# Performance work log

Hardware: AMD Instinct MI355X
Metric: run time of the kernel (lower is better)

The kernel has to match this reference:

```python
import jax, jax.numpy as jnp
import numpy as np

N = 1_000_000   # total points
C = 20          # semantic classes
B = 4           # scenes in batch
L = 200         # instance label vocabulary
INST = 64       # number of proposals/instances
M = 300_000     # masked points (len(object_idxs))
T = 320_000     # total proposal rows
IGNORE = -100
PREPARE_EPOCHS = 128


def setup_inputs() -> dict:
    key = jax.random.key(0)
    ks = jax.random.split(key, 12)
    semantic_scores = jax.random.normal(ks[0], (N, C), jnp.float32)
    semantic_labels = jax.random.randint(ks[1], (N,), 0, C)
    lab = jax.random.randint(ks[2], (N,), 0, L)
    ign = jax.random.uniform(ks[3], (N,)) < 0.05
    instance_labels = jnp.where(ign, IGNORE, lab)
    pt_offsets = jax.random.normal(ks[4], (N, 3), jnp.float32)
    instance_info = jax.random.normal(ks[5], (N, 9), jnp.float32)
    coords = jax.random.normal(ks[6], (N, 3), jnp.float32)
    mask_logits = jax.random.normal(ks[7], (INST, M), jnp.float32)
    object_idxs = jax.random.randint(ks[8], (M,), 0, N)
    col1 = jax.random.randint(ks[9], (T,), 0, N)
    proposals_idx_shift = jnp.stack([jnp.zeros_like(col1), col1], axis=1)
    mids = jnp.sort(jax.random.randint(ks[10], (INST - 1,), 0, T))
    proposals_offset_shift = jnp.concatenate(
        [jnp.zeros((1,), jnp.int32), mids.astype(jnp.int32), jnp.full((1,), T, jnp.int32)])
    inst_batch_ids = jax.random.randint(ks[11], (INST,), 0, B)
    batch_offsets = jnp.array([0, N // 4, N // 2, 3 * N // 4, N], dtype=jnp.int32)
    batch_ids = jnp.clip(jnp.searchsorted(batch_offsets, object_idxs, side='right') - 1, 0, B - 1)
    inst_pred_seg_label = jax.random.randint(jax.random.fold_in(key, 99), (INST,), 0, C)
    return dict(semantic_scores=semantic_scores, pt_offsets=pt_offsets,
                instance_info=instance_info, coords=coords, mask_logits=mask_logits,
                semantic_labels=semantic_labels, instance_labels=instance_labels,
                object_idxs=object_idxs, proposals_idx_shift=proposals_idx_shift,
                proposals_offset_shift=proposals_offset_shift, inst_batch_ids=inst_batch_ids,
                batch_ids=batch_ids, batch_offsets=batch_offsets,
                inst_pred_seg_label=inst_pred_seg_label, epoch=200)


def reference(semantic_scores, pt_offsets, instance_info, coords, mask_logits,
              semantic_labels, instance_labels, object_idxs, proposals_idx_shift,
              proposals_offset_shift, inst_batch_ids, batch_ids, batch_offsets,
              inst_pred_seg_label, epoch):
    f32 = jnp.float32
    n_pts = semantic_scores.shape[0]
    n_inst, m_pts = mask_logits.shape
    n_batch = batch_offsets.shape[0] - 1
    LW = L + 1  # label buckets, bucket 0 == ignore(-100)

    # --- semantic cross entropy (ignore_index) ---
    logp = jax.nn.log_softmax(semantic_scores, axis=-1)
    sem_valid = semantic_labels != IGNORE
    safe_lab = jnp.where(sem_valid, semantic_labels, 0)
    nll = -jnp.take_along_axis(logp, safe_lab[:, None], axis=1)[:, 0]
    semantic_loss = jnp.sum(nll * sem_valid) / jnp.maximum(jnp.sum(sem_valid), 1)

    # --- offset losses ---
    gt_offsets = instance_info[:, 0:3] - coords
    pt_dist = jnp.sum(jnp.abs(pt_offsets - gt_offsets), axis=-1)
    valid = (instance_labels != IGNORE).astype(f32)
    vsum = jnp.sum(valid) + 1e-6
    offset_norm_loss = jnp.sum(pt_dist * valid) / vsum
    gt_u = gt_offsets / (jnp.linalg.norm(gt_offsets, axis=1, keepdims=True) + 1e-8)
    pt_u = pt_offsets / (jnp.linalg.norm(pt_offsets, axis=1, keepdims=True) + 1e-8)
    offset_dir_loss = jnp.sum(-jnp.sum(gt_u * pt_u, axis=-1) * valid) / vsum

    loss = semantic_loss + offset_norm_loss + offset_dir_loss

    if epoch > PREPARE_EPOCHS:
        # map instance labels to ids: ignore -> 0, label l -> l+1 (order-preserving, so
        # argmax-first tie-break == torch.mode smallest-value tie-break)
        labels_id = jnp.where(instance_labels == IGNORE, 0, instance_labels + 1)
        # segment id per proposal row from CSR offsets
        seg = jnp.clip(jnp.searchsorted(proposals_offset_shift, jnp.arange(T), side='right') - 1,
                       0, n_inst - 1)
        prop_lab = labels_id[proposals_idx_shift[:, 1]]
        hist = jax.ops.segment_sum(jnp.ones((T,), f32), seg * LW + prop_lab,
                                   num_segments=n_inst * LW).reshape(n_inst, LW)
        mode_id = jnp.argmax(hist, axis=1)                       # [INST] per-instance mode vote

        masked_lab = labels_id[object_idxs]                      # [M]
        sem_masked = semantic_labels[object_idxs]                # [M]
        skip = (mode_id == 0) | (inst_pred_seg_label <= 3)       # [INST]

        batch_match = inst_batch_ids[:, None] == batch_ids[None, :]           # [INST,M]
        sem_match = inst_pred_seg_label[:, None] == sem_masked[None, :]       # [INST,M]
        weights = batch_match.astype(f32) * jnp.where(skip[:, None], 1.0,
                                                      sem_match.astype(f32))  # [INST,M]

        # per-batch label histograms (full points and masked points)
        point_batch = jnp.clip(jnp.searchsorted(batch_offsets, jnp.arange(n_pts),
                                                side='right') - 1, 0, n_batch - 1)
        hist_full = jax.ops.segment_sum(jnp.ones((n_pts,), f32), point_batch * LW + labels_id,
                                        num_segments=n_batch * LW).reshape(n_batch, LW)
        hist_mask = jax.ops.segment_sum(jnp.ones((m_pts,), f32), batch_ids * LW + masked_lab,
                                        num_segments=n_batch * LW).reshape(n_batch, LW)
        num = hist_mask[inst_batch_ids, mode_id]
        den = hist_full[inst_batch_ids, mode_id]
        cover = jnp.where(den > 0, num / den, 0.0)
        pos = (~skip) & (cover > 0.3)
        inst_gt_mask = (pos[:, None] & (masked_lab[None, :] == mode_id[:, None])).astype(f32)

        pred = jax.nn.sigmoid(mask_logits)
        wb = (weights > 0).astype(f32)
        inter = jnp.sum(wb * pred * inst_gt_mask, axis=1)
        union = jnp.sum(wb * pred * pred, axis=1) + jnp.sum(wb * inst_gt_mask * inst_gt_mask, axis=1) + 1e-5
        dice_n = 1.0 - 2.0 * inter / union
        dice_valid = (~skip) & (jnp.sum(wb, axis=1) > 0)
        dice_loss = jnp.sum(jnp.where(dice_valid, dice_n, 0.0)) / (jnp.sum(dice_valid.astype(f32)) + 1e-6)

        # BCE(sigmoid(x), t) in stable form: softplus(x) - t*x
        bce = jax.nn.softplus(mask_logits) - inst_gt_mask * mask_logits
        score_loss = jnp.sum(bce * weights) / (jnp.sum(weights) + 1e-6)

        loss = loss + score_loss + dice_loss
    return loss
```

## Files before the change

kernel.cpp:

```cpp
#include <hip/hip_runtime.h>
#include <math.h>

namespace {

constexpr int N_PTS  = 1000000;
constexpr int C_CLS  = 20;
constexpr int N_B    = 4;
constexpr int L_LAB  = 200;
constexpr int LW     = L_LAB + 1;
constexpr int N_INST = 64;
constexpr int M_PTS  = 300000;
constexpr int T_PROP = 320000;
constexpr int IGN    = -100;
constexpr int PREP   = 128;

constexpr size_t OFF_G      = 0;
constexpr size_t OFF_INTER  = 64;
constexpr size_t OFF_UP     = 576;
constexpr size_t OFF_UG     = 1088;
constexpr size_t OFF_WBS    = 1600;
constexpr size_t OFF_SN     = 2112;
constexpr size_t OFF_HFULL  = 2624;
constexpr size_t OFF_HMASK  = 5840;
constexpr size_t OFF_IHIST  = 9056;
constexpr size_t OFF_FLAGS  = 60512;
constexpr size_t ZERO_BYTES = 60768;
constexpr size_t OFF_META   = 60800;
constexpr size_t WS_REQUIRED = OFF_META + (size_t)M_PTS * 2;

__device__ __forceinline__ float waveSumF(float v) {
  #pragma unroll
  for (int off = 32; off > 0; off >>= 1) v += __shfl_down(v, off, 64);
  return v;
}
__device__ __forceinline__ int waveMaxI(int v) {
  #pragma unroll
  for (int off = 32; off > 0; off >>= 1) v = max(v, __shfl_down(v, off, 64));
  return v;
}

constexpr int PB_PT   = 1024;
constexpr int PB_HF   = 256;
constexpr int PB_PROP = 256;
constexpr int PB_HM   = 256;
constexpr int A_BLOCKS = PB_PT + PB_HF + PB_PROP + PB_HM;

__global__ __launch_bounds__(256) void k_A(const float* __restrict__ scores,
                                           const float* __restrict__ pt_off,
                                           const float* __restrict__ info,
                                           const float* __restrict__ coords,
                                           const int* __restrict__ sem_lab,
                                           const int* __restrict__ inst_lab,
                                           const int* __restrict__ obj_idx,
                                           const int* __restrict__ batch_ids,
                                           const int* __restrict__ prop_idx,
                                           const int* __restrict__ prop_off,
                                           const int* __restrict__ batch_off,
                                           double* __restrict__ g,
                                           int* __restrict__ hist_full,
                                           int* __restrict__ hist_mask,
                                           int* __restrict__ inst_hist,
                                           unsigned short* __restrict__ meta,
                                           int write_meta) {
  __shared__ int sh[N_B * LW];
  const int bx = blockIdx.x;

  if (bx < PB_PT) {
    float s_nll = 0.f, s_cnt = 0.f, s_dist = 0.f, s_dir = 0.f, s_val = 0.f;
    const int gid = bx * blockDim.x + threadIdx.x;
    const int p0  = gid * 4;
    if (p0 < N_PTS) {
      const int4 sl4 = *reinterpret_cast<const int4*>(sem_lab + p0);
      const int4 il4 = *reinterpret_cast<const int4*>(inst_lab + p0);
      const float4* c4 = reinterpret_cast<const float4*>(coords + (size_t)p0 * 3);
      const float4 ca = c4[0], cb = c4[1], cc = c4[2];
      const float4* o4 = reinterpret_cast<const float4*>(pt_off + (size_t)p0 * 3);
      const float4 oa = o4[0], ob = o4[1], oc = o4[2];
      const float4* i4 = reinterpret_cast<const float4*>(info + (size_t)p0 * 9);
      const float4 f0 = i4[0], f2 = i4[2], f4 = i4[4], f5 = i4[5], f6 = i4[6], f7 = i4[7];
      const float cx[4] = { ca.x, ca.w, cb.z, cc.y };
      const float cy[4] = { ca.y, cb.x, cb.w, cc.z };
      const float cz[4] = { ca.z, cb.y, cc.x, cc.w };
      const float ox[4] = { oa.x, oa.w, ob.z, oc.y };
      const float oy[4] = { oa.y, ob.x, ob.w, oc.z };
      const float oz[4] = { oa.z, ob.y, oc.x, oc.w };
      const float ix[4] = { f0.x, f2.y, f4.z, f6.w };
      const float iy[4] = { f0.y, f2.z, f4.w, f7.x };
      const float iz[4] = { f0.z, f2.w, f5.x, f7.y };
      const int sl[4] = { sl4.x, sl4.y, sl4.z, sl4.w };
      const int il[4] = { il4.x, il4.y, il4.z, il4.w };
      #pragma unroll
      for (int k = 0; k < 4; ++k) {
        const int p = p0 + k;
        const float4* r4 = reinterpret_cast<const float4*>(scores + (size_t)p * C_CLS);
        float x[C_CLS];
        #pragma unroll
        for (int q = 0; q < C_CLS / 4; ++q) {
          const float4 v = r4[q];
          x[4 * q + 0] = v.x; x[4 * q + 1] = v.y; x[4 * q + 2] = v.z; x[4 * q + 3] = v.w;
        }
        float mx = x[0];
        #pragma unroll
        for (int c = 1; c < C_CLS; ++c) mx = fmaxf(mx, x[c]);
        float se = 0.f;
        #pragma unroll
        for (int c = 0; c < C_CLS; ++c) se += __expf(x[c] - mx);
        const float lse = mx + __logf(se);
        if (sl[k] != IGN) { s_nll += lse - x[sl[k]]; s_cnt += 1.f; }
        const float gx = ix[k] - cx[k];
        const float gy = iy[k] - cy[k];
        const float gz = iz[k] - cz[k];
        if (il[k] != IGN) {
          s_val  += 1.f;
          s_dist += fabsf(ox[k] - gx) + fabsf(oy[k] - gy) + fabsf(oz[k] - gz);
          const float gn = sqrtf(gx * gx + gy * gy + gz * gz) + 1e-8f;
          const float pn = sqrtf(ox[k] * ox[k] + oy[k] * oy[k] + oz[k] * oz[k]) + 1e-8f;
          s_dir += -((gx * ox[k] + gy * oy[k] + gz * oz[k]) / (gn * pn));
        }
      }
    }
    float* red = reinterpret_cast<float*>(sh);
    float vals[5] = { s_nll, s_cnt, s_dist, s_dir, s_val };
    const int lane = threadIdx.x & 63, wv = threadIdx.x >> 6;
    #pragma unroll
    for (int k = 0; k < 5; ++k) {
      const float t = waveSumF(vals[k]);
      if (lane == 0) red[k * 4 + wv] = t;
    }
    __syncthreads();
    if (threadIdx.x < 5) {
      const float s = red[threadIdx.x * 4 + 0] + red[threadIdx.x * 4 + 1] +
                      red[threadIdx.x * 4 + 2] + red[threadIdx.x * 4 + 3];
      atomicAdd(&g[threadIdx.x], (double)s);
    }
  } else if (bx < PB_PT + PB_HF) {
    for (int t = threadIdx.x; t < N_B * LW; t += blockDim.x) sh[t] = 0;
    __syncthreads();
    const int b1 = batch_off[1], b2 = batch_off[2], b3 = batch_off[3];
    const int blk = bx - PB_PT;
    const int4* il4p = reinterpret_cast<const int4*>(inst_lab);
    const int nq = N_PTS / 4;
    for (int q = blk * blockDim.x + threadIdx.x; q < nq; q += PB_HF * blockDim.x) {
      const int4 v = il4p[q];
      const int p = q * 4;
      const int ils[4] = { v.x, v.y, v.z, v.w };
      #pragma unroll
      for (int k = 0; k < 4; ++k) {
        const int lab = (ils[k] == IGN) ? 0 : (ils[k] + 1);
        const int pp = p + k;
        int pb = 0;
        if (pp >= b1) pb = 1;
        if (pp >= b2) pb = 2;
        if (pp >= b3) pb = 3;
        atomicAdd(&sh[pb * LW + lab], 1);
      }
    }
    __syncthreads();
    for (int t = threadIdx.x; t < N_B * LW; t += blockDim.x)
      if (sh[t]) atomicAdd(&hist_full[t], sh[t]);
  } else if (bx < PB_PT + PB_HF + PB_PROP) {
    if (threadIdx.x <= N_INST) sh[threadIdx.x] = prop_off[threadIdx.x];
    __syncthreads();
    const int blk = bx - PB_PT - PB_HF;
    const int4* pi4 = reinterpret_cast<const int4*>(prop_idx);
    const int nq = T_PROP / 2;
    for (int q = blk * blockDim.x + threadIdx.x; q < nq; q += PB_PROP * blockDim.x) {
      const int4 v = pi4[q];
      const int t0 = 2 * q, t1 = 2 * q + 1;
      const int il0 = inst_lab[v.y];
      const int il1 = inst_lab[v.w];
      int lo0 = 0, hi0 = N_INST + 1, lo1 = 0, hi1 = N_INST + 1;
      #pragma unroll
      for (int s = 0; s < 7; ++s) {
        const int m0 = (lo0 + hi0) >> 1;
        if (m0 <= N_INST && sh[m0] <= t0) lo0 = m0 + 1; else hi0 = m0;
        const int m1 = (lo1 + hi1) >> 1;
        if (m1 <= N_INST && sh[m1] <= t1) lo1 = m1 + 1; else hi1 = m1;
      }
      const int seg0 = min(lo0 - 1, N_INST - 1);
      const int seg1 = min(lo1 - 1, N_INST - 1);
      const int lab0 = (il0 == IGN) ? 0 : (il0 + 1);
      const int lab1 = (il1 == IGN) ? 0 : (il1 + 1);
      atomicAdd(&inst_hist[seg0 * LW + lab0], 1);
      atomicAdd(&inst_hist[seg1 * LW + lab1], 1);
    }
  } else {
    for (int t = threadIdx.x; t < N_B * LW; t += blockDim.x) sh[t] = 0;
    __syncthreads();
    const int blk = bx - PB_PT - PB_HF - PB_PROP;
    const int4* oi4 = reinterpret_cast<const int4*>(obj_idx);
    const int4* bi4 = reinterpret_cast<const int4*>(batch_ids);
    ushort4* m4 = reinterpret_cast<ushort4*>(meta);
    const int nq = M_PTS / 4;
    for (int q = blk * blockDim.x + threadIdx.x; q < nq; q += PB_HM * blockDim.x) {
      const int4 o = oi4[q];
      const int4 b = bi4[q];
      const int il0 = inst_lab[o.x], il1 = inst_lab[o.y],
                il2 = inst_lab[o.z], il3 = inst_lab[o.w];
      const int sm0 = sem_lab[o.x], sm1 = sem_lab[o.y],
                sm2 = sem_lab[o.z], sm3 = sem_lab[o.w];
      const int ml0 = (il0 == IGN) ? 0 : (il0 + 1);
      const int ml1 = (il1 == IGN) ? 0 : (il1 + 1);
      const int ml2 = (il2 == IGN) ? 0 : (il2 + 1);
      const int ml3 = (il3 == IGN) ? 0 : (il3 + 1);
      atomicAdd(&sh[b.x * LW + ml0], 1);
      atomicAdd(&sh[b.y * LW + ml1], 1);
      atomicAdd(&sh[b.z * LW + ml2], 1);
      atomicAdd(&sh[b.w * LW + ml3], 1);
      if (write_meta) {
        ushort4 mm;
        mm.x = (unsigned short)(ml0 | (sm0 << 8) | (b.x << 13));
        mm.y = (unsigned short)(ml1 | (sm1 << 8) | (b.y << 13));
        mm.z = (unsigned short)(ml2 | (sm2 << 8) | (b.z << 13));
        mm.w = (unsigned short)(ml3 | (sm3 << 8) | (b.w << 13));
        m4[q] = mm;
      }
    }
    __syncthreads();
    for (int t = threadIdx.x; t < N_B * LW; t += blockDim.x)
      if (sh[t]) atomicAdd(&hist_mask[t], sh[t]);
  }
}

__global__ __launch_bounds__(256) void k_argmax(const int* __restrict__ inst_hist,
                                                const int* __restrict__ hist_full,
                                                const int* __restrict__ hist_mask,
                                                const int* __restrict__ inst_batch_ids,
                                                const int* __restrict__ inst_seg,
                                                int* __restrict__ flags) {
  __shared__ int red[4];
  const int i = blockIdx.x;
  const int t = threadIdx.x;
  int key = 0;
  if (t < LW) {
    const int cnt = inst_hist[i * LW + t];
    key = (cnt << 8) | (255 - t);
  }
  key = waveMaxI(key);
  const int lane = t & 63, wv = t >> 6;
  if (lane == 0) red[wv] = key;
  __syncthreads();
  if (t == 0) {
    int k = max(max(red[0], red[1]), max(red[2], red[3]));
    const int m = 255 - (k & 0xFF);
    const int b = inst_batch_ids[i];
    const int seg = inst_seg[i];
    const bool skip = (m == 0) || (seg <= 3);
    const float num = (float)hist_mask[b * LW + m];
    const float den = (float)hist_full[b * LW + m];
    const float cover = (den > 0.f) ? (num / den) : 0.f;
    const bool pos = (!skip) && (cover > 0.3f);
    flags[i] = m | (skip ? 0x100 : 0) | (pos ? 0x200 : 0) | (b << 10) | (seg << 12);
  }
}

template <bool USE_META>
__global__ __launch_bounds__(256) void k_mask(const float* __restrict__ logits,
                                              const unsigned short* __restrict__ meta,
                                              const int* __restrict__ obj_idx,
                                              const int* __restrict__ inst_lab,
                                              const int* __restrict__ sem_lab,
                                              const int* __restrict__ batch_ids,
                                              const int* __restrict__ flags,
                                              double* __restrict__ i_inter,
                                              double* __restrict__ i_up,
                                              double* __restrict__ i_ug,
                                              double* __restrict__ i_wbs,
                                              double* __restrict__ i_sn) {
  const int i  = blockIdx.y;
  const int fl = flags[i];
  const int  mode_i = fl & 0xFF;
  const bool skip   = (fl >> 8) & 1;
  const bool pos    = (fl >> 9) & 1;
  const int  bi     = (fl >> 10) & 3;
  const int  seg    = (fl >> 12) & 31;

  float inter = 0.f, up = 0.f, ug = 0.f, wbs = 0.f, sn = 0.f;

  if (USE_META) {
    const float4* row4 = reinterpret_cast<const float4*>(logits + (size_t)i * M_PTS);
    const ushort4* m4  = reinterpret_cast<const ushort4*>(meta);
    const int nq = M_PTS / 4;
    for (int q = blockIdx.x * blockDim.x + threadIdx.x; q < nq; q += gridDim.x * blockDim.x) {
      const float4  x4 = row4[q];
      const ushort4 d4 = m4[q];
      const float xs[4] = { x4.x, x4.y, x4.z, x4.w };
      const int   ds[4] = { d4.x, d4.y, d4.z, d4.w };
      #pragma unroll
      for (int k = 0; k < 4; ++k) {
        const int md = ds[k];
        const int ml = md & 0xFF;
        const int sm = (md >> 8) & 31;
        const int b  = (md >> 13) & 3;
        const bool w  = (b == bi) && (skip || (sm == seg));
        const bool gt = pos && (ml == mode_i);
        const float x  = xs[k];
        const float e  = __expf(-fabsf(x));
        const float r  = __builtin_amdgcn_rcpf(1.f + e);
        const float pr = (x >= 0.f) ? r : e * r;
        const float sp = fmaxf(x, 0.f) + __logf(1.f + e);
        const float wf = w ? 1.f : 0.f;
        const float gf = gt ? 1.f : 0.f;
        up    += wf * pr * pr;
        wbs   += wf;
        sn    += wf * (sp - gf * x);
        inter += wf * gf * pr;
        ug    += wf * gf;
      }
    }
  } else {
    const float* row = logits + (size_t)i * M_PTS;
    for (int j = blockIdx.x * blockDim.x + threadIdx.x; j < M_PTS; j += gridDim.x * blockDim.x) {
      const int o  = obj_idx[j];
      const int il = inst_lab[o];
      const int ml = (il == IGN) ? 0 : (il + 1);
      const int sm = sem_lab[o];
      const int b  = batch_ids[j];
      const bool w  = (b == bi) && (skip || (sm == seg));
      const bool gt = pos && (ml == mode_i);
      const float x  = row[j];
      const float e  = __expf(-fabsf(x));
      const float r  = __builtin_amdgcn_rcpf(1.f + e);
      const float pr = (x >= 0.f) ? r : e * r;
      const float sp = fmaxf(x, 0.f) + __logf(1.f + e);
      const float wf = w ? 1.f : 0.f;
      const float gf = gt ? 1.f : 0.f;
      up    += wf * pr * pr;
      wbs   += wf;
      sn    += wf * (sp - gf * x);
      inter += wf * gf * pr;
      ug    += wf * gf;
    }
  }

  __shared__ float red[5][4];
  float vals[5] = { inter, up, ug, wbs, sn };
  const int lane = threadIdx.x & 63, wv = threadIdx.x >> 6;
  #pragma unroll
  for (int k = 0; k < 5; ++k) {
    const float t = waveSumF(vals[k]);
    if (lane == 0) red[k][wv] = t;
  }
  __syncthreads();
  if (threadIdx.x < 5) {
    const float s = red[threadIdx.x][0] + red[threadIdx.x][1] + red[threadIdx.x][2] + red[threadIdx.x][3];
    double* dst = (threadIdx.x == 0) ? (i_inter + i)
                : (threadIdx.x == 1) ? (i_up + i)
                : (threadIdx.x == 2) ? (i_ug + i)
                : (threadIdx.x == 3) ? (i_wbs + i)
                                     : (i_sn + i);
    atomicAdd(dst, (double)s);
  }
}

__global__ void k_final(const double* __restrict__ g,
                        const double* __restrict__ i_inter,
                        const double* __restrict__ i_up,
                        const double* __restrict__ i_ug,
                        const double* __restrict__ i_wbs,
                        const double* __restrict__ i_sn,
                        const int* __restrict__ flags,
                        const int* __restrict__ epoch,
                        float* __restrict__ out) {
  if (threadIdx.x != 0 || blockIdx.x != 0) return;
  double loss = g[0] / fmax(g[1], 1.0);
  const double vsum = g[4] + 1e-6;
  loss += g[2] / vsum + g[3] / vsum;
  if (epoch[0] > PREP) {
    double sn = 0.0, wsum = 0.0, dice = 0.0, dcnt = 0.0;
    for (int i = 0; i < N_INST; ++i) {
      wsum += i_wbs[i];
      sn   += i_sn[i];
      const bool skip = (flags[i] >> 8) & 1;
      if (!skip && i_wbs[i] > 0.0) {
        const double un = i_up[i] + i_ug[i] + 1e-5;
        dice += 1.0 - 2.0 * i_inter[i] / un;
        dcnt += 1.0;
      }
    }
    loss += sn / (wsum + 1e-6) + dice / (dcnt + 1e-6);
  }
  out[0] = (float)loss;
}

}

extern "C" void kernel_launch(void* const* d_in, const int* in_sizes, int n_in,
                              void* d_out, int out_size, void* d_ws, size_t ws_size,
                              hipStream_t stream) {
  const float* semantic_scores  = (const float*)d_in[0];
  const float* pt_offsets       = (const float*)d_in[1];
  const float* instance_info    = (const float*)d_in[2];
  const float* coords           = (const float*)d_in[3];
  const float* mask_logits      = (const float*)d_in[4];
  const int*   semantic_labels  = (const int*)d_in[5];
  const int*   instance_labels  = (const int*)d_in[6];
  const int*   object_idxs      = (const int*)d_in[7];
  const int*   proposals_idx    = (const int*)d_in[8];
  const int*   proposals_off    = (const int*)d_in[9];
  const int*   inst_batch_ids   = (const int*)d_in[10];
  const int*   batch_ids        = (const int*)d_in[11];
  const int*   batch_offsets    = (const int*)d_in[12];
  const int*   inst_seg         = (const int*)d_in[13];
  const int*   epoch            = (const int*)d_in[14];
  float* out = (float*)d_out;

  char* w = (char*)d_ws;
  double* g        = (double*)(w + OFF_G);
  double* i_inter  = (double*)(w + OFF_INTER);
  double* i_up     = (double*)(w + OFF_UP);
  double* i_ug     = (double*)(w + OFF_UG);
  double* i_wbs    = (double*)(w + OFF_WBS);
  double* i_sn     = (double*)(w + OFF_SN);
  int* hist_full   = (int*)(w + OFF_HFULL);
  int* hist_mask   = (int*)(w + OFF_HMASK);
  int* inst_hist   = (int*)(w + OFF_IHIST);
  int* flags       = (int*)(w + OFF_FLAGS);
  unsigned short* meta = (unsigned short*)(w + OFF_META);

  const bool use_meta = (ws_size >= WS_REQUIRED);

  (void)hipMemsetAsync(d_ws, 0, ZERO_BYTES, stream);

  k_A<<<A_BLOCKS, 256, 0, stream>>>(semantic_scores, pt_offsets, instance_info, coords,
                                    semantic_labels, instance_labels, object_idxs,
                                    batch_ids, proposals_idx, proposals_off, batch_offsets,
                                    g, hist_full, hist_mask, inst_hist, meta,
                                    use_meta ? 1 : 0);

  k_argmax<<<N_INST, 256, 0, stream>>>(inst_hist, hist_full, hist_mask,
                                       inst_batch_ids, inst_seg, flags);

  dim3 mgrid(40, N_INST);
  if (use_meta) {
    k_mask<true><<<mgrid, 256, 0, stream>>>(mask_logits, meta, object_idxs, instance_labels,
                                            semantic_labels, batch_ids, flags,
                                            i_inter, i_up, i_ug, i_wbs, i_sn);
  } else {
    k_mask<false><<<mgrid, 256, 0, stream>>>(mask_logits, meta, object_idxs, instance_labels,
                                             semantic_labels, batch_ids, flags,
                                             i_inter, i_up, i_ug, i_wbs, i_sn);
  }
  k_final<<<1, 64, 0, stream>>>(g, i_inter, i_up, i_ug, i_wbs, i_sn, flags, epoch, out);
}
```

Measured before the change: 296.9 us.

## Stage point data through per-wave LDS tiles for coalesced loads; parallelize final reduction

The per-point loss blocks now process 64-point tiles per wave in a grid-stride loop. Scores, coords, offsets and instance info are loaded into shared memory with fully coalesced float4 reads and then read transposed per lane. Previously each thread loaded strided per-point rows directly. The final kernel is rewritten to reduce the 64 instance terms with wave shuffles instead of a single serial thread. The cost is extra block-wide barriers per tile and a larger shared buffer, which may reduce occupancy.

New measurement: 273.7 us. 7.8% less time.

```diff
diff --git a/kernel.cpp b/kernel.cpp
--- a/kernel.cpp
+++ b/kernel.cpp
@@ -62,75 +62,91 @@
                                            int* __restrict__ inst_hist,
                                            unsigned short* __restrict__ meta,
                                            int write_meta) {
-  __shared__ int sh[N_B * LW];
+  __shared__ float4 shbuf4[4 * 320];
+  int*   sh  = reinterpret_cast<int*>(shbuf4);
+  float* shf = reinterpret_cast<float*>(shbuf4);
   const int bx = blockIdx.x;
 
   if (bx < PB_PT) {
+    const int lane = threadIdx.x & 63, wv = threadIdx.x >> 6;
+    float4* shw4 = shbuf4 + wv * 320;
+    float*  shwf = reinterpret_cast<float*>(shw4);
     float s_nll = 0.f, s_cnt = 0.f, s_dist = 0.f, s_dir = 0.f, s_val = 0.f;
-    const int gid = bx * blockDim.x + threadIdx.x;
-    const int p0  = gid * 4;
-    if (p0 < N_PTS) {
-      const int4 sl4 = *reinterpret_cast<const int4*>(sem_lab + p0);
-      const int4 il4 = *reinterpret_cast<const int4*>(inst_lab + p0);
-      const float4* c4 = reinterpret_cast<const float4*>(coords + (size_t)p0 * 3);
-      const float4 ca = c4[0], cb = c4[1], cc = c4[2];
-      const float4* o4 = reinterpret_cast<const float4*>(pt_off + (size_t)p0 * 3);
-      const float4 oa = o4[0], ob = o4[1], oc = o4[2];
-      const float4* i4 = reinterpret_cast<const float4*>(info + (size_t)p0 * 9);
-      const float4 f0 = i4[0], f2 = i4[2], f4 = i4[4], f5 = i4[5], f6 = i4[6], f7 = i4[7];
-      const float cx[4] = { ca.x, ca.w, cb.z, cc.y };
-      const float cy[4] = { ca.y, cb.x, cb.w, cc.z };
-      const float cz[4] = { ca.z, cb.y, cc.x, cc.w };
-      const float ox[4] = { oa.x, oa.w, ob.z, oc.y };
-      const float oy[4] = { oa.y, ob.x, ob.w, oc.z };
-      const float oz[4] = { oa.z, ob.y, oc.x, oc.w };
-      const float ix[4] = { f0.x, f2.y, f4.z, f6.w };
-      const float iy[4] = { f0.y, f2.z, f4.w, f7.x };
-      const float iz[4] = { f0.z, f2.w, f5.x, f7.y };
-      const int sl[4] = { sl4.x, sl4.y, sl4.z, sl4.w };
-      const int il[4] = { il4.x, il4.y, il4.z, il4.w };
-      #pragma unroll
-      for (int k = 0; k < 4; ++k) {
-        const int p = p0 + k;
-        const float4* r4 = reinterpret_cast<const float4*>(scores + (size_t)p * C_CLS);
-        float x[C_CLS];
+
+    constexpr int NT      = N_PTS / 64;
+    constexpr int TSTRIDE = PB_PT * 4;
+    const int base = bx * 4 + wv;
+    const int nit = (NT - bx * 4 + TSTRIDE - 1) / TSTRIDE;
+
+    for (int it = 0; it < nit; ++it) {
+      const int tile = base + it * TSTRIDE;
+      const bool act = tile < NT;
+      int sl = 0, il = IGN;
+
+      if (act) {
+        const int p = tile * 64 + lane;
+        sl = sem_lab[p];
+        il = inst_lab[p];
+        const float4* s4 = reinterpret_cast<const float4*>(scores) + (size_t)tile * 320;
         #pragma unroll
-        for (int q = 0; q < C_CLS / 4; ++q) {
-          const float4 v = r4[q];
-          x[4 * q + 0] = v.x; x[4 * q + 1] = v.y; x[4 * q + 2] = v.z; x[4 * q + 3] = v.w;
+        for (int r = 0; r < 5; ++r) shw4[r * 64 + lane] = s4[r * 64 + lane];
+      }
+      __syncthreads();
+
+      if (act) {
+        float mx = -3.4e38f;
+        #pragma unroll
+        for (int r = 0; r < 5; ++r) {
+          const float4 a = shw4[lane * 5 + r];
+          mx = fmaxf(mx, fmaxf(fmaxf(a.x, a.y), fmaxf(a.z, a.w)));
         }
-        float mx = x[0];
-        #pragma unroll
-        for (int c = 1; c < C_CLS; ++c) mx = fmaxf(mx, x[c]);
         float se = 0.f;
         #pragma unroll
-        for (int c = 0; c < C_CLS; ++c) se += __expf(x[c] - mx);
-        const float lse = mx + __logf(se);
-        if (sl[k] != IGN) { s_nll += lse - x[sl[k]]; s_cnt += 1.f; }
-        const float gx = ix[k] - cx[k];
-        const float gy = iy[k] - cy[k];
-        const float gz = iz[k] - cz[k];
-        if (il[k] != IGN) {
-          s_val  += 1.f;
-          s_dist += fabsf(ox[k] - gx) + fabsf(oy[k] - gy) + fabsf(oz[k] - gz);
-          const float gn = sqrtf(gx * gx + gy * gy + gz * gz) + 1e-8f;
-          const float pn = sqrtf(ox[k] * ox[k] + oy[k] * oy[k] + oz[k] * oz[k]) + 1e-8f;
-          s_dir += -((gx * ox[k] + gy * oy[k] + gz * oz[k]) / (gn * pn));
+        for (int r = 0; r < 5; ++r) {
+          const float4 a = shw4[lane * 5 + r];
+          se += __expf(a.x - mx) + __expf(a.y - mx) + __expf(a.z - mx) + __expf(a.w - mx);
         }
-      }
-    }
-    float* red = reinterpret_cast<float*>(sh);
+        const float xs = shwf[lane * 20 + ((sl == IGN) ? 0 : sl)];
+        if (sl != IGN) { s_nll += (mx + __logf(se)) - xs; s_cnt += 1.f; }
+      }
+      __syncthreads();
+
+      if (act) {
+        const float4* c4 = reinterpret_cast<const float4*>(coords) + (size_t)tile * 48;
+        const float4* o4 = reinterpret_cast<const float4*>(pt_off) + (size_t)tile * 48;
+        const float4* i4 = reinterpret_cast<const float4*>(info)   + (size_t)tile * 144;
+        if (lane < 48) { shw4[lane] = c4[lane]; shw4[48 + lane] = o4[lane]; }
+        shw4[96 + lane]  = i4[lane];
+        shw4[160 + lane] = i4[64 + lane];
+        if (lane < 16) shw4[224 + lane] = i4[128 + lane];
+      }
+      __syncthreads();
+
+      if (act && il != IGN) {
+        const float cx = shwf[3 * lane + 0], cy = shwf[3 * lane + 1], cz = shwf[3 * lane + 2];
+        const float ox = shwf[192 + 3 * lane + 0], oy = shwf[192 + 3 * lane + 1], oz = shwf[192 + 3 * lane + 2];
+        const float gx = shwf[384 + 9 * lane + 0] - cx;
+        const float gy = shwf[384 + 9 * lane + 1] - cy;
+        const float gz = shwf[384 + 9 * lane + 2] - cz;
+        s_val  += 1.f;
+        s_dist += fabsf(ox - gx) + fabsf(oy - gy) + fabsf(oz - gz);
+        const float gn = sqrtf(gx * gx + gy * gy + gz * gz) + 1e-8f;
+        const float pn = sqrtf(ox * ox + oy * oy + oz * oz) + 1e-8f;
+        s_dir += -((gx * ox + gy * oy + gz * oz) / (gn * pn));
+      }
+      __syncthreads();
+    }
+
     float vals[5] = { s_nll, s_cnt, s_dist, s_dir, s_val };
-    const int lane = threadIdx.x & 63, wv = threadIdx.x >> 6;
     #pragma unroll
     for (int k = 0; k < 5; ++k) {
       const float t = waveSumF(vals[k]);
-      if (lane == 0) red[k * 4 + wv] = t;
+      if (lane == 0) shf[k * 4 + wv] = t;
     }
     __syncthreads();
     if (threadIdx.x < 5) {
-      const float s = red[threadIdx.x * 4 + 0] + red[threadIdx.x * 4 + 1] +
-                      red[threadIdx.x * 4 + 2] + red[threadIdx.x * 4 + 3];
+      const float s = shf[threadIdx.x * 4 + 0] + shf[threadIdx.x * 4 + 1] +
+                      shf[threadIdx.x * 4 + 2] + shf[threadIdx.x * 4 + 3];
       atomicAdd(&g[threadIdx.x], (double)s);
     }
   } else if (bx < PB_PT + PB_HF) {
@@ -353,34 +369,42 @@
   }
 }
 
-__global__ void k_final(const double* __restrict__ g,
-                        const double* __restrict__ i_inter,
-                        const double* __restrict__ i_up,
-                        const double* __restrict__ i_ug,
-                        const double* __restrict__ i_wbs,
-                        const double* __restrict__ i_sn,
-                        const int* __restrict__ flags,
-                        const int* __restrict__ epoch,
-                        float* __restrict__ out) {
-  if (threadIdx.x != 0 || blockIdx.x != 0) return;
-  double loss = g[0] / fmax(g[1], 1.0);
-  const double vsum = g[4] + 1e-6;
-  loss += g[2] / vsum + g[3] / vsum;
-  if (epoch[0] > PREP) {
-    double sn = 0.0, wsum = 0.0, dice = 0.0, dcnt = 0.0;
-    for (int i = 0; i < N_INST; ++i) {
-      wsum += i_wbs[i];
-      sn   += i_sn[i];
-      const bool skip = (flags[i] >> 8) & 1;
-      if (!skip && i_wbs[i] > 0.0) {
-        const double un = i_up[i] + i_ug[i] + 1e-5;
-        dice += 1.0 - 2.0 * i_inter[i] / un;
-        dcnt += 1.0;
-      }
-    }
-    loss += sn / (wsum + 1e-6) + dice / (dcnt + 1e-6);
-  }
-  out[0] = (float)loss;
+__global__ __launch_bounds__(64) void k_final(const double* __restrict__ g,
+                                              const double* __restrict__ i_inter,
+                                              const double* __restrict__ i_up,
+                                              const double* __restrict__ i_ug,
+                                              const double* __restrict__ i_wbs,
+                                              const double* __restrict__ i_sn,
+                                              const int* __restrict__ flags,
+                                              const int* __restrict__ epoch,
+                                              float* __restrict__ out) {
+  const int i = threadIdx.x;
+  const bool act = epoch[0] > PREP;
+  double sn = 0.0, wsum = 0.0, dice = 0.0, dcnt = 0.0;
+  if (act) {
+    wsum = i_wbs[i];
+    sn   = i_sn[i];
+    const bool skip = (flags[i] >> 8) & 1;
+    if (!skip && wsum > 0.0) {
+      const double un = i_up[i] + i_ug[i] + 1e-5;
+      dice = 1.0 - 2.0 * i_inter[i] / un;
+      dcnt = 1.0;
+    }
+    #pragma unroll
+    for (int off = 32; off > 0; off >>= 1) {
+      wsum += __shfl_down(wsum, off, 64);
+      sn   += __shfl_down(sn,   off, 64);
+      dice += __shfl_down(dice, off, 64);
+      dcnt += __shfl_down(dcnt, off, 64);
+    }
+  }
+  if (i == 0) {
+    double loss = g[0] / fmax(g[1], 1.0);
+    const double vsum = g[4] + 1e-6;
+    loss += g[2] / vsum + g[3] / vsum;
+    if (act) loss += sn / (wsum + 1e-6) + dice / (dcnt + 1e-6);
+    out[0] = (float)loss;
+  }
 }
 
 }
```
